# Kernel optimization log

Measured on AMD Instinct MI355X. Metric: run time of the kernel, lower is better.

Reference implementation:

```python
import jax, jax.numpy as jnp
import numpy as np

GRID_SIZE = 8
SPLINE_ORDER = 3
LAYERS = [256, 512, 512, 256]  # [input_dim] + hidden_dims
BATCH = 8192
BN_EPS = 1e-5


def make_grid(in_features):
    # efficient-kan/torchkan grid: uniform on [-1, 1] extended by spline_order on each side
    h = 2.0 / GRID_SIZE
    g = jnp.arange(-SPLINE_ORDER, GRID_SIZE + SPLINE_ORDER + 1, dtype=jnp.float32) * h - 1.0
    return jnp.broadcast_to(g, (in_features, g.shape[0]))  # (In, G + 2k + 1)


def b_splines(x, grid):
    # x: (B, In), grid: (In, G + 2k + 1) -> bases: (B, In, G + k)
    xg = x[:, :, None]
    bases = ((xg >= grid[:, :-1]) & (xg < grid[:, 1:])).astype(x.dtype)
    for k in range(1, SPLINE_ORDER + 1):
        left = (xg - grid[:, : -(k + 1)]) / (grid[:, k:-1] - grid[:, : -(k + 1)])
        right = (grid[:, k + 1 :] - xg) / (grid[:, k + 1 :] - grid[:, 1:-k])
        bases = left * bases[:, :, :-1] + right * bases[:, :, 1:]
    return bases


def kan_linear(x, grid, base_w, spline_w):
    # base path: GELU (exact, matching torch.nn.GELU) then linear
    base_out = jax.nn.gelu(x, approximate=False) @ base_w.T
    spline_out = jnp.einsum('bik,oik->bo', b_splines(x, grid), spline_w)
    return base_out + spline_out


def setup_inputs() -> dict:
    key = jax.random.key(0)
    ks = jax.random.split(key, 16)
    inp = {'x': jax.random.normal(ks[0], (BATCH, LAYERS[0]), dtype=jnp.float32)}
    n_bases = GRID_SIZE + SPLINE_ORDER
    for i, (fin, fout) in enumerate(zip(LAYERS[:-1], LAYERS[1:])):
        scale = 1.0 / np.sqrt(fin)
        inp[f'grid{i}'] = make_grid(fin)
        inp[f'base_w{i}'] = jax.random.normal(ks[1 + 3 * i], (fout, fin), dtype=jnp.float32) * scale
        inp[f'spline_w{i}'] = jax.random.normal(ks[2 + 3 * i], (fout, fin, n_bases), dtype=jnp.float32) * (0.1 * scale)
    d_out = LAYERS[-1]
    inp['bn_gamma'] = jnp.ones((d_out,), dtype=jnp.float32)
    inp['bn_beta'] = jnp.zeros((d_out,), dtype=jnp.float32)
    inp['bn_mean'] = jax.random.normal(ks[10], (d_out,), dtype=jnp.float32) * 0.1
    inp['bn_var'] = jax.random.uniform(ks[11], (d_out,), dtype=jnp.float32, minval=0.5, maxval=1.5)
    return inp


def reference(x, grid0, base_w0, spline_w0, grid1, base_w1, spline_w1, grid2, base_w2, spline_w2, bn_gamma, bn_beta, bn_mean, bn_var):
    h = kan_linear(x, grid0, base_w0, spline_w0)
    h = kan_linear(h, grid1, base_w1, spline_w1)
    h = kan_linear(h, grid2, base_w2, spline_w2)
    # BatchNorm1d in eval mode (running stats); Dropout is identity at inference
    return bn_gamma * (h - bn_mean) * jax.lax.rsqrt(bn_var + BN_EPS) + bn_beta
```

## Files before the change

kernel.cpp:

```cpp
#include <hip/hip_runtime.h>
#include <hip/hip_bf16.h>
#include <cstdint>


typedef unsigned short ushort_t;
typedef __bf16 bf16x8 __attribute__((ext_vector_type(8)));
typedef float f32x4 __attribute__((ext_vector_type(4)));

__device__ __forceinline__ ushort_t f2bf(float f) {
    __bf16 h = (__bf16)f;
    return __builtin_bit_cast(ushort_t, h);
}
__device__ __forceinline__ float bf2f(ushort_t u) {
    unsigned int v = ((unsigned int)u) << 16;
    return __builtin_bit_cast(float, v);
}

__device__ __forceinline__ void gload_lds16(const void* g, void* lds) {
    __builtin_amdgcn_global_load_lds(
        (const __attribute__((address_space(1))) unsigned int*)(uintptr_t)g,
        (__attribute__((address_space(3))) unsigned int*)(unsigned int)(uintptr_t)lds,
        16, 0, 0);
}

__device__ __forceinline__ void expand12(float x, ushort_t* o) {
    float x3 = x * x * x;
    float y  = 0.7978845608028654f * (x + 0.044715f * x3);
    float e  = __expf(2.0f * y);
    float th = 1.0f - 2.0f / (e + 1.0f);
    o[0] = f2bf(0.5f * x * (1.0f + th));
    float xs = (x + 1.75f) * 4.0f;
#pragma unroll
    for (int j = 0; j < 11; ++j) {
        float t  = xs - (float)j;
        float a  = fabsf(t - 2.0f);
        float p1 = (3.0f * a - 6.0f) * a * a + 4.0f;
        float c  = 2.0f - a;
        float p2 = c * c * c;
        float v  = (a <= 1.0f) ? p1 : fmaxf(p2, 0.0f);
        o[1 + j] = f2bf(v * (1.0f / 6.0f));
    }
}

__global__ __launch_bounds__(256) void prep_kernel(
    const float* __restrict__ bw0, const float* __restrict__ sw0, ushort_t* __restrict__ W0,
    const float* __restrict__ bw1, const float* __restrict__ sw1, ushort_t* __restrict__ W1,
    const float* __restrict__ bw2, const float* __restrict__ sw2, ushort_t* __restrict__ W2,
    const float* __restrict__ x, ushort_t* __restrict__ A)
{
    int b = blockIdx.x;
    if (b < 2048) {
        int idx = b * 256 + threadIdx.x;
        const float* bw; const float* sw; ushort_t* W; int local;
        if (idx < 131072)      { bw = bw0; sw = sw0; W = W0; local = idx; }
        else if (idx < 393216) { bw = bw1; sw = sw1; W = W1; local = idx - 131072; }
        else                   { bw = bw2; sw = sw2; W = W2; local = idx - 393216; }
        union { ushort_t us[12]; uint2 v[3]; } pk;
        pk.us[0] = f2bf(bw[local]);
        const float* s = sw + (size_t)local * 11;
#pragma unroll
        for (int k = 0; k < 11; ++k) pk.us[1 + k] = f2bf(s[k]);
        uint2* dst = (uint2*)(W + (size_t)local * 12);
        dst[0] = pk.v[0]; dst[1] = pk.v[1]; dst[2] = pk.v[2];
    } else {
        int idx = (b - 2048) * 256 + threadIdx.x;
        float4 h = *(const float4*)(x + 4 * (size_t)idx);
        union { ushort_t us[48]; uint4 v[6]; } pk;
        expand12(h.x, pk.us);
        expand12(h.y, pk.us + 12);
        expand12(h.z, pk.us + 24);
        expand12(h.w, pk.us + 36);
        uint4* dst = (uint4*)(A + (size_t)idx * 48);
#pragma unroll
        for (int j = 0; j < 6; ++j) dst[j] = pk.v[j];
    }
}

__global__ __launch_bounds__(256) void expand_kernel(
    const ushort_t* __restrict__ P, size_t stride,
    ushort_t* __restrict__ A, int total4)
{
    int idx = blockIdx.x * 256 + threadIdx.x;
    if (idx >= total4) return;
    float h[4] = {0.f, 0.f, 0.f, 0.f};
#pragma unroll
    for (int z = 0; z < 4; ++z) {
        ushort4 p = *(const ushort4*)(P + z * stride + 4 * (size_t)idx);
        h[0] += bf2f(p.x); h[1] += bf2f(p.y); h[2] += bf2f(p.z); h[3] += bf2f(p.w);
    }
    union { ushort_t us[48]; uint4 v[6]; } pk;
    expand12(h[0], pk.us);
    expand12(h[1], pk.us + 12);
    expand12(h[2], pk.us + 24);
    expand12(h[3], pk.us + 36);
    uint4* dst = (uint4*)(A + (size_t)idx * 48);
#pragma unroll
    for (int j = 0; j < 6; ++j) dst[j] = pk.v[j];
}

__global__ __launch_bounds__(512, 4) void gemm_kernel(
    const ushort_t* __restrict__ A,
    const ushort_t* __restrict__ W,
    ushort_t* __restrict__ C,
    int M, int N, int K, int kcps)
{
    __shared__ __align__(16) ushort_t As[256 * 64];
    __shared__ __align__(16) ushort_t Bs[128 * 64];

    const int t   = threadIdx.x;
    const int l   = t & 63;
    const int w   = t >> 6;
    const int wm  = w >> 1;
    const int wn  = w & 1;
    const int l15 = l & 15;
    const int q   = l >> 4;
    const int blockM = blockIdx.x * 256;
    const int blockN = blockIdx.y * 128;
    const int kb0 = blockIdx.z * kcps, kb1 = kb0 + kcps;
    ushort_t* Cz = C + (size_t)blockIdx.z * M * N;

    f32x4 acc[4][4];
#pragma unroll
    for (int i = 0; i < 4; ++i)
#pragma unroll
        for (int j = 0; j < 4; ++j) acc[i][j] = (f32x4){0.f, 0.f, 0.f, 0.f};

    for (int kb = kb0; kb < kb1; ++kb) {
        const int k0 = kb << 6;
#pragma unroll
        for (int it = 0; it < 4; ++it) {
            int s   = it * 512 + t;
            int row = s >> 3, c = s & 7;
            int g   = c ^ (row & 7);
            gload_lds16(A + ((size_t)(blockM + row) * K + k0 + g * 8), &As[s * 8]);
        }
#pragma unroll
        for (int it = 0; it < 2; ++it) {
            int s   = it * 512 + t;
            int row = s >> 3, c = s & 7;
            int g   = c ^ (row & 7);
            gload_lds16(W + ((size_t)(blockN + row) * K + k0 + g * 8), &Bs[s * 8]);
        }
        __syncthreads();

#pragma unroll
        for (int ks = 0; ks < 2; ++ks) {
            const int kc = ks * 4 + q;
            bf16x8 af[4], bf[4];
#pragma unroll
            for (int mi = 0; mi < 4; ++mi) {
                int m  = wm * 64 + mi * 16 + l15;
                int cs = kc ^ (m & 7);
                af[mi] = *(const bf16x8*)&As[(size_t)(m * 8 + cs) * 8];
            }
#pragma unroll
            for (int ni = 0; ni < 4; ++ni) {
                int n  = wn * 64 + ni * 16 + l15;
                int cs = kc ^ (n & 7);
                bf[ni] = *(const bf16x8*)&Bs[(size_t)(n * 8 + cs) * 8];
            }
#pragma unroll
            for (int mi = 0; mi < 4; ++mi)
#pragma unroll
                for (int ni = 0; ni < 4; ++ni)
                    acc[mi][ni] = __builtin_amdgcn_mfma_f32_16x16x32_bf16(
                        af[mi], bf[ni], acc[mi][ni], 0, 0, 0);
        }
        __syncthreads();
    }

#pragma unroll
    for (int ni = 0; ni < 4; ++ni) {
        int n = blockN + wn * 64 + ni * 16 + l15;
#pragma unroll
        for (int mi = 0; mi < 4; ++mi) {
            int mb = blockM + wm * 64 + mi * 16 + q * 4;
#pragma unroll
            for (int r = 0; r < 4; ++r)
                Cz[(size_t)(mb + r) * N + n] = f2bf(acc[mi][ni][r]);
        }
    }
}

__global__ __launch_bounds__(256) void bn_reduce_kernel(
    const ushort_t* __restrict__ P, size_t stride,
    const float* __restrict__ gamma, const float* __restrict__ beta,
    const float* __restrict__ mean,  const float* __restrict__ var,
    float4* __restrict__ out, int n4)
{
    int i = blockIdx.x * 256 + threadIdx.x;
    if (i >= n4) return;
    float h[4] = {0.f, 0.f, 0.f, 0.f};
#pragma unroll
    for (int z = 0; z < 8; ++z) {
        ushort4 p = *(const ushort4*)(P + z * stride + 4 * (size_t)i);
        h[0] += bf2f(p.x); h[1] += bf2f(p.y); h[2] += bf2f(p.z); h[3] += bf2f(p.w);
    }
    int nb = (i * 4) & 255;
    float4 g  = *(const float4*)(gamma + nb);
    float4 be = *(const float4*)(beta + nb);
    float4 mn = *(const float4*)(mean + nb);
    float4 vr = *(const float4*)(var + nb);
    float4 o;
    o.x = g.x * rsqrtf(vr.x + 1e-5f) * (h[0] - mn.x) + be.x;
    o.y = g.y * rsqrtf(vr.y + 1e-5f) * (h[1] - mn.y) + be.y;
    o.z = g.z * rsqrtf(vr.z + 1e-5f) * (h[2] - mn.z) + be.z;
    o.w = g.w * rsqrtf(vr.w + 1e-5f) * (h[3] - mn.w) + be.w;
    out[i] = o;
}

extern "C" void kernel_launch(void* const* d_in, const int* in_sizes, int n_in,
                              void* d_out, int out_size, void* d_ws, size_t ws_size,
                              hipStream_t stream) {
    const float* x     = (const float*)d_in[0];
    const float* bw0   = (const float*)d_in[2];
    const float* sw0   = (const float*)d_in[3];
    const float* bw1   = (const float*)d_in[5];
    const float* sw1   = (const float*)d_in[6];
    const float* bw2   = (const float*)d_in[8];
    const float* sw2   = (const float*)d_in[9];
    const float* gamma = (const float*)d_in[10];
    const float* beta  = (const float*)d_in[11];
    const float* mean  = (const float*)d_in[12];
    const float* var   = (const float*)d_in[13];

    char* ws = (char*)d_ws;
    ushort_t* Abuf = (ushort_t*)(ws);
    ushort_t* W0   = (ushort_t*)(ws + 100663296);
    ushort_t* W1   = (ushort_t*)(ws + 103809024);
    ushort_t* W2   = (ushort_t*)(ws + 110100480);
    ushort_t* P    = (ushort_t*)(ws + 113246208);
    float*    out  = (float*)d_out;

    const size_t PS = (size_t)8192 * 512;
    const size_t QS = (size_t)8192 * 256;

    prep_kernel<<<4096, 256, 0, stream>>>(bw0, sw0, W0, bw1, sw1, W1,
                                          bw2, sw2, W2, x, Abuf);
    {
        dim3 g(32, 4, 4);
        gemm_kernel<<<g, 512, 0, stream>>>(Abuf, W0, P, 8192, 512, 3072, 12);
    }
    expand_kernel<<<4096, 256, 0, stream>>>(P, PS, Abuf, 8192 * 512 / 4);
    {
        dim3 g(32, 4, 4);
        gemm_kernel<<<g, 512, 0, stream>>>(Abuf, W1, P, 8192, 512, 6144, 24);
    }
    expand_kernel<<<4096, 256, 0, stream>>>(P, PS, Abuf, 8192 * 512 / 4);
    {
        dim3 g(32, 2, 8);
        gemm_kernel<<<g, 512, 0, stream>>>(Abuf, W2, P, 8192, 256, 6144, 12);
    }
    bn_reduce_kernel<<<2048, 256, 0, stream>>>(P, QS, gamma, beta, mean, var,
                                               (float4*)out, 8192 * 256 / 4);
}
```

Measured before the change: 308.9 us.

## Store expanded activations in K-chunk-major layout for contiguous GEMM tile loads

The expanded spline/GELU activation buffer moves from row-major (M x K) to a K-chunk-major layout where each 8-element K chunk is stored contiguously across all M rows. The GEMM A-tile loads then read consecutive rows of one K chunk from contiguous memory, and the expand kernels are reorganized so each thread handles one row and writes 16-byte chunks. This is meant to improve coalescing of the GEMM's A global-to-LDS loads. In exchange, the expand writes become strided per feature pair, which may cost store efficiency.

```diff
diff --git a/kernel.cpp b/kernel.cpp
--- a/kernel.cpp
+++ b/kernel.cpp
@@ -6,6 +6,8 @@
 typedef unsigned short ushort_t;
 typedef __bf16 bf16x8 __attribute__((ext_vector_type(8)));
 typedef float f32x4 __attribute__((ext_vector_type(4)));
+
+#define MROWS 8192
 
 __device__ __forceinline__ ushort_t f2bf(float f) {
     __bf16 h = (__bf16)f;
@@ -39,6 +41,38 @@
         float p2 = c * c * c;
         float v  = (a <= 1.0f) ? p1 : fmaxf(p2, 0.0f);
         o[1 + j] = f2bf(v * (1.0f / 6.0f));
+    }
+}
+
+template <bool SUM>
+__device__ __forceinline__ void expand_body(
+    const float* __restrict__ Xf, const ushort_t* __restrict__ Pb, size_t stride,
+    ushort_t* __restrict__ A, int fin, int mb, int fpg, int l, int w)
+{
+    const int m   = mb * 64 + l;
+    const int fp0 = fpg * 64 + w * 16;
+    const size_t rowoff = (size_t)m * fin;
+#pragma unroll 4
+    for (int i = 0; i < 16; ++i) {
+        int fp = fp0 + i;
+        float h0, h1;
+        if (SUM) {
+            h0 = 0.f; h1 = 0.f;
+#pragma unroll
+            for (int z = 0; z < 4; ++z) {
+                ushort2 p = *(const ushort2*)(Pb + z * stride + rowoff + 2 * fp);
+                h0 += bf2f(p.x); h1 += bf2f(p.y);
+            }
+        } else {
+            float2 hv = *(const float2*)(Xf + rowoff + 2 * fp);
+            h0 = hv.x; h1 = hv.y;
+        }
+        union { ushort_t us[24]; uint4 v[3]; } pk;
+        expand12(h0, pk.us);
+        expand12(h1, pk.us + 12);
+#pragma unroll
+        for (int j = 0; j < 3; ++j)
+            *(uint4*)(A + ((size_t)(3 * fp + j) * MROWS + m) * 8) = pk.v[j];
     }
 }
 
@@ -63,39 +97,19 @@
         uint2* dst = (uint2*)(W + (size_t)local * 12);
         dst[0] = pk.v[0]; dst[1] = pk.v[1]; dst[2] = pk.v[2];
     } else {
-        int idx = (b - 2048) * 256 + threadIdx.x;
-        float4 h = *(const float4*)(x + 4 * (size_t)idx);
-        union { ushort_t us[48]; uint4 v[6]; } pk;
-        expand12(h.x, pk.us);
-        expand12(h.y, pk.us + 12);
-        expand12(h.z, pk.us + 24);
-        expand12(h.w, pk.us + 36);
-        uint4* dst = (uint4*)(A + (size_t)idx * 48);
-#pragma unroll
-        for (int j = 0; j < 6; ++j) dst[j] = pk.v[j];
+        int bx  = b - 2048;
+        int mb  = bx >> 1;
+        int fpg = bx & 1;
+        expand_body<false>(x, nullptr, 0, A, 256, mb, fpg,
+                           threadIdx.x & 63, threadIdx.x >> 6);
     }
 }
 
 __global__ __launch_bounds__(256) void expand_kernel(
-    const ushort_t* __restrict__ P, size_t stride,
-    ushort_t* __restrict__ A, int total4)
-{
-    int idx = blockIdx.x * 256 + threadIdx.x;
-    if (idx >= total4) return;
-    float h[4] = {0.f, 0.f, 0.f, 0.f};
-#pragma unroll
-    for (int z = 0; z < 4; ++z) {
-        ushort4 p = *(const ushort4*)(P + z * stride + 4 * (size_t)idx);
-        h[0] += bf2f(p.x); h[1] += bf2f(p.y); h[2] += bf2f(p.z); h[3] += bf2f(p.w);
-    }
-    union { ushort_t us[48]; uint4 v[6]; } pk;
-    expand12(h[0], pk.us);
-    expand12(h[1], pk.us + 12);
-    expand12(h[2], pk.us + 24);
-    expand12(h[3], pk.us + 36);
-    uint4* dst = (uint4*)(A + (size_t)idx * 48);
-#pragma unroll
-    for (int j = 0; j < 6; ++j) dst[j] = pk.v[j];
+    const ushort_t* __restrict__ P, size_t stride, ushort_t* __restrict__ A)
+{
+    expand_body<true>(nullptr, P, stride, A, 512, blockIdx.x, blockIdx.y,
+                      threadIdx.x & 63, threadIdx.x >> 6);
 }
 
 __global__ __launch_bounds__(512, 4) void gemm_kernel(
@@ -132,7 +146,7 @@
             int s   = it * 512 + t;
             int row = s >> 3, c = s & 7;
             int g   = c ^ (row & 7);
-            gload_lds16(A + ((size_t)(blockM + row) * K + k0 + g * 8), &As[s * 8]);
+            gload_lds16(A + ((size_t)(kb * 8 + g) * M + blockM + row) * 8, &As[s * 8]);
         }
 #pragma unroll
         for (int it = 0; it < 2; ++it) {
@@ -235,18 +249,24 @@
     const size_t PS = (size_t)8192 * 512;
     const size_t QS = (size_t)8192 * 256;
 
-    prep_kernel<<<4096, 256, 0, stream>>>(bw0, sw0, W0, bw1, sw1, W1,
+    prep_kernel<<<2304, 256, 0, stream>>>(bw0, sw0, W0, bw1, sw1, W1,
                                           bw2, sw2, W2, x, Abuf);
     {
         dim3 g(32, 4, 4);
         gemm_kernel<<<g, 512, 0, stream>>>(Abuf, W0, P, 8192, 512, 3072, 12);
     }
-    expand_kernel<<<4096, 256, 0, stream>>>(P, PS, Abuf, 8192 * 512 / 4);
+    {
+        dim3 g(128, 4);
+        expand_kernel<<<g, 256, 0, stream>>>(P, PS, Abuf);
+    }
     {
         dim3 g(32, 4, 4);
         gemm_kernel<<<g, 512, 0, stream>>>(Abuf, W1, P, 8192, 512, 6144, 24);
     }
-    expand_kernel<<<4096, 256, 0, stream>>>(P, PS, Abuf, 8192 * 512 / 4);
+    {
+        dim3 g(128, 4);
+        expand_kernel<<<g, 256, 0, stream>>>(P, PS, Abuf);
+    }
     {
         dim3 g(32, 2, 8);
         gemm_kernel<<<g, 512, 0, stream>>>(Abuf, W2, P, 8192, 256, 6144, 12);
```

Measured after the change: 434.6 us. +40.7%, slower.
